# Optimization experiments

Measured on AMD Instinct MI355X. Metric: run time of the kernel, lower is better.

## Reference

```python
import jax, jax.numpy as jnp
import numpy as np

Bsz, L, D, N = 2, 2048, 1024, 16
LN_EPS = 1e-5


def setup_inputs() -> dict:
    key = jax.random.key(0)
    ks = jax.random.split(key, 5)
    # A_log initialized as in the module: -log(arange(1, N+1)) broadcast over D
    A_log = -jnp.broadcast_to(jnp.log(jnp.arange(1, N + 1, dtype=jnp.float32))[None, :], (D, N))
    return {
        "x": jax.random.normal(ks[0], (Bsz, L, D), jnp.float32),
        "W_dt": jax.random.normal(ks[1], (D, D), jnp.float32) * 0.02,
        "b_dt": jnp.zeros((D,), jnp.float32),
        "W_B": jax.random.normal(ks[2], (N, D), jnp.float32) * 0.02,
        "W_C": jax.random.normal(ks[3], (N, D), jnp.float32) * 0.02,
        "D_param": jnp.ones((D,), jnp.float32),
        "A_log": A_log,
        "gamma": jnp.ones((D,), jnp.float32),
        "beta": jnp.zeros((D,), jnp.float32),
    }


def reference(x, W_dt, b_dt, W_B, W_C, D_param, A_log, gamma, beta):
    residual = x
    # LayerNorm (biased variance, eps=1e-5)
    mu = jnp.mean(x, axis=-1, keepdims=True)
    var = jnp.var(x, axis=-1, keepdims=True)
    xn = (x - mu) * jax.lax.rsqrt(var + LN_EPS) * gamma + beta

    dt = jax.nn.softplus(xn @ W_dt.T + b_dt)          # (B, L, D)
    A = -jnp.exp(A_log)                                # (D, N)
    B_in = xn @ W_B.T                                  # (B, L, N)
    C_in = xn @ W_C.T                                  # (B, L, N)

    A_bar = jnp.exp(dt[..., None] * A)                 # (B, L, D, N)
    # B_bar[t] * x[t] fused: dt * B_in * xn -> (B, L, D, N)
    Bx = dt[..., None] * B_in[:, :, None, :] * xn[..., None]

    def step(h, inputs):
        a_t, bx_t, c_t = inputs                        # (B,D,N), (B,D,N), (B,N)
        h = a_t * h + bx_t                             # (B, D, N)
        y_t = jnp.einsum('bn,bdn->bd', c_t, h)         # (B, D)
        return h, y_t

    h0 = jnp.zeros((x.shape[0], D, N), x.dtype)
    _, ys = jax.lax.scan(
        step, h0,
        (jnp.transpose(A_bar, (1, 0, 2, 3)),
         jnp.transpose(Bx, (1, 0, 2, 3)),
         jnp.transpose(C_in, (1, 0, 2))))
    y = jnp.transpose(ys, (1, 0, 2)) + D_param * residual
    return y
```

## Files before the change

### kernel.cpp

```cpp
#include <hip/hip_runtime.h>
#include <cstddef>

#define Bsz 2
#define Lr  2048
#define Dr  1024
#define Nr  16
#define M_ROWS (Bsz*Lr)
#define NPAD   1088
#define CHUNK  16
#define NCH    (Lr/CHUNK)

#define BM 64
#define BN 64
#define BK 64
#define NK (Dr/BK)

typedef __attribute__((ext_vector_type(8))) __bf16 bf16x8;
typedef __attribute__((ext_vector_type(4))) float floatx4;

__device__ __forceinline__ unsigned short f2bf(float f) {
    unsigned u = __float_as_uint(f);
    u += 0x7fffu + ((u >> 16) & 1u);
    return (unsigned short)(u >> 16);
}

__device__ __forceinline__ float bf2f(unsigned short u) {
    return __uint_as_float(((unsigned)u) << 16);
}

__device__ __forceinline__ float softplus_f(float x) {
    if (x > 0.f) return x + __logf(1.f + __expf(-x));
    return __logf(1.f + __expf(x));
}

__device__ __forceinline__ void gload_lds16(const unsigned short* g, unsigned short* l) {
    __builtin_amdgcn_global_load_lds((const __attribute__((address_space(1))) void*)g,
                                     (__attribute__((address_space(3))) void*)l, 16, 0, 0);
}

__global__ __launch_bounds__(256) void ln_pack_kernel(const float* __restrict__ x,
                                                      const float* __restrict__ gamma,
                                                      const float* __restrict__ beta,
                                                      unsigned short* __restrict__ xnb,
                                                      const float* __restrict__ Wdt,
                                                      const float* __restrict__ WB,
                                                      const float* __restrict__ WC,
                                                      unsigned short* __restrict__ Wcat) {
    if (blockIdx.x >= M_ROWS) {
        int i = (blockIdx.x - M_ROWS) * 256 + threadIdx.x;
        int row = i >> 10;
        int col = i & 1023;
        float v;
        if (row < Dr)                 v = Wdt[i];
        else if (row < Dr + Nr)       v = WB[(row - Dr) * Dr + col];
        else if (row < Dr + 2*Nr)     v = WC[(row - Dr - Nr) * Dr + col];
        else                          v = 0.f;
        Wcat[i] = f2bf(v);
        return;
    }
    int row = blockIdx.x;
    int tid = threadIdx.x;
    const float4* xr = (const float4*)(x + (size_t)row * Dr);
    float4 v = xr[tid];
    float s  = v.x + v.y + v.z + v.w;
    float ss = v.x*v.x + v.y*v.y + v.z*v.z + v.w*v.w;
    #pragma unroll
    for (int off = 32; off > 0; off >>= 1) {
        s  += __shfl_down(s, off);
        ss += __shfl_down(ss, off);
    }
    __shared__ float red[8];
    int wid = tid >> 6;
    if ((tid & 63) == 0) { red[wid*2] = s; red[wid*2+1] = ss; }
    __syncthreads();
    if (tid == 0) {
        float S = 0.f, SS = 0.f;
        #pragma unroll
        for (int w = 0; w < 4; w++) { S += red[w*2]; SS += red[w*2+1]; }
        float mu  = S * (1.f/Dr);
        float var = SS * (1.f/Dr) - mu*mu;
        red[0] = mu;
        red[1] = rsqrtf(var + 1e-5f);
    }
    __syncthreads();
    float mu = red[0], rs = red[1];
    float4 g = ((const float4*)gamma)[tid], bt = ((const float4*)beta)[tid];
    float4 o;
    o.x = (v.x - mu) * rs * g.x + bt.x;
    o.y = (v.y - mu) * rs * g.y + bt.y;
    o.z = (v.z - mu) * rs * g.z + bt.z;
    o.w = (v.w - mu) * rs * g.w + bt.w;
    ushort4 ob;
    ob.x = f2bf(o.x); ob.y = f2bf(o.y); ob.z = f2bf(o.z); ob.w = f2bf(o.w);
    ((ushort4*)(xnb + (size_t)row * Dr))[tid] = ob;
}

__global__ __launch_bounds__(256) void gemm_kernel(const unsigned short* __restrict__ xnb,
                                                   const unsigned short* __restrict__ w,
                                                   const float* __restrict__ b_dt,
                                                   unsigned short* __restrict__ dt,
                                                   float* __restrict__ bin,
                                                   float* __restrict__ cin) {
    __shared__ unsigned short As[BM * BK];
    __shared__ unsigned short Bs[BN * BK];
    int tid  = threadIdx.x;
    int wave = tid >> 6;
    int lane = tid & 63;
    int lm   = lane & 15;
    int quad = lane >> 4;
    int bid  = blockIdx.x;
    int xcd  = bid & 7;
    int j0   = bid >> 3;
    int nt   = j0 % 17;
    int mt   = (j0 / 17) * 8 + xcd;
    int Mb = mt * BM;
    int Nb = nt * BN;
    int wm = (wave >> 1) * 32;
    int wn = (wave & 1)  * 32;
    int koff = (mt + nt) & (NK - 1);

    int r0 = tid >> 3,         cg0 = (tid & 7) ^ (r0 & 7);
    int r1 = (tid + 256) >> 3, cg1 = ((tid + 256) & 7) ^ (r1 & 7);
    const unsigned short* Ag0 = xnb + (size_t)(Mb + r0) * Dr + cg0 * 8;
    const unsigned short* Ag1 = xnb + (size_t)(Mb + r1) * Dr + cg1 * 8;
    const unsigned short* Bg0 = w   + (size_t)(Nb + r0) * Dr + cg0 * 8;
    const unsigned short* Bg1 = w   + (size_t)(Nb + r1) * Dr + cg1 * 8;
    unsigned short* Al0 = &As[(size_t)tid * 8];
    unsigned short* Al1 = &As[(size_t)(tid + 256) * 8];
    unsigned short* Bl0 = &Bs[(size_t)tid * 8];
    unsigned short* Bl1 = &Bs[(size_t)(tid + 256) * 8];

    floatx4 acc[2][2] = {};

    for (int kk = 0; kk < NK; kk++) {
        int k0 = ((kk + koff) & (NK - 1)) * BK;
        gload_lds16(Ag0 + k0, Al0);
        gload_lds16(Ag1 + k0, Al1);
        gload_lds16(Bg0 + k0, Bl0);
        gload_lds16(Bg1 + k0, Bl1);
        __syncthreads();
        #pragma unroll
        for (int s = 0; s < 2; s++) {
            int ra0 = wm + lm, ra1 = wm + 16 + lm;
            int rb0 = wn + lm, rb1 = wn + 16 + lm;
            int cg = s * 4 + quad;
            bf16x8 a0 = *(const bf16x8*)&As[ra0 * BK + ((cg ^ (ra0 & 7)) * 8)];
            bf16x8 a1 = *(const bf16x8*)&As[ra1 * BK + ((cg ^ (ra1 & 7)) * 8)];
            bf16x8 b0 = *(const bf16x8*)&Bs[rb0 * BK + ((cg ^ (rb0 & 7)) * 8)];
            bf16x8 b1 = *(const bf16x8*)&Bs[rb1 * BK + ((cg ^ (rb1 & 7)) * 8)];
            acc[0][0] = __builtin_amdgcn_mfma_f32_16x16x32_bf16(a0, b0, acc[0][0], 0, 0, 0);
            acc[0][1] = __builtin_amdgcn_mfma_f32_16x16x32_bf16(a0, b1, acc[0][1], 0, 0, 0);
            acc[1][0] = __builtin_amdgcn_mfma_f32_16x16x32_bf16(a1, b0, acc[1][0], 0, 0, 0);
            acc[1][1] = __builtin_amdgcn_mfma_f32_16x16x32_bf16(a1, b1, acc[1][1], 0, 0, 0);
        }
        __syncthreads();
    }

    #pragma unroll
    for (int i = 0; i < 2; i++) {
        int grow0 = Mb + wm + i * 16 + quad * 4;
        #pragma unroll
        for (int jj = 0; jj < 2; jj++) {
            int gcol = Nb + wn + jj * 16 + lm;
            #pragma unroll
            for (int r = 0; r < 4; r++) {
                float v = acc[i][jj][r];
                int row = grow0 + r;
                if (gcol < Dr) {
                    dt[(size_t)row * Dr + gcol] = f2bf(softplus_f(v + b_dt[gcol]));
                } else if (gcol < Dr + Nr) {
                    bin[(size_t)row * Nr + (gcol - Dr)] = v;
                } else if (gcol < Dr + 2*Nr) {
                    cin[(size_t)row * Nr + (gcol - Dr - Nr)] = v;
                }
            }
        }
    }
}

__global__ __launch_bounds__(256) void scan1_kernel(const unsigned short* __restrict__ dtb,
                                                    const unsigned short* __restrict__ xnb,
                                                    const float* __restrict__ bin,
                                                    const float* __restrict__ A_log,
                                                    unsigned short* __restrict__ Pws,
                                                    unsigned short* __restrict__ hendws) {
    int tid = threadIdx.x;
    int d  = blockIdx.x * 256 + tid;
    int ch = blockIdx.y;
    int b  = blockIdx.z;
    size_t rowbase = (size_t)b * Lr + ch * CHUNK;

    float ac[16];
    #pragma unroll
    for (int i = 0; i < 4; i++) {
        float4 t = ((const float4*)(A_log + (size_t)d * Nr))[i];
        ac[i*4+0] = -__expf(t.x);
        ac[i*4+1] = -__expf(t.y);
        ac[i*4+2] = -__expf(t.z);
        ac[i*4+3] = -__expf(t.w);
    }

    __shared__ float lb[CHUNK * Nr];
    lb[tid] = bin[rowbase * Nr + tid];
    __syncthreads();

    float dtv[CHUNK], xv[CHUNK];
    {
        const unsigned short* dtp = dtb + rowbase * Dr + d;
        const unsigned short* xp  = xnb + rowbase * Dr + d;
        #pragma unroll
        for (int t = 0; t < CHUNK; t++) {
            dtv[t] = bf2f(dtp[(size_t)t * Dr]);
            xv[t]  = bf2f(xp[(size_t)t * Dr]);
        }
    }

    float h[16];
    #pragma unroll
    for (int n = 0; n < 16; n++) h[n] = 0.f;
    float S = 0.f;

    #pragma unroll
    for (int t = 0; t < CHUNK; t++) {
        float dv = dtv[t];
        S += dv;
        float cm = dv * xv[t];
        const float4* br4 = (const float4*)(lb + t * Nr);
        float4 q0 = br4[0], q1 = br4[1], q2 = br4[2], q3 = br4[3];
        float bb[16] = {q0.x,q0.y,q0.z,q0.w, q1.x,q1.y,q1.z,q1.w,
                        q2.x,q2.y,q2.z,q2.w, q3.x,q3.y,q3.z,q3.w};
        #pragma unroll
        for (int n = 0; n < 16; n++)
            h[n] = __expf(dv * ac[n]) * h[n] + cm * bb[n];
    }

    size_t obase = ((size_t)(b * NCH + ch) * Nr) * Dr + d;
    #pragma unroll
    for (int n = 0; n < 16; n++) {
        Pws[obase + (size_t)n * Dr]    = f2bf(__expf(S * ac[n]));
        hendws[obase + (size_t)n * Dr] = f2bf(h[n]);
    }
}

__global__ __launch_bounds__(256) void combine_kernel(const unsigned short* __restrict__ Pws,
                                                      const unsigned short* __restrict__ hendws,
                                                      unsigned short* __restrict__ hinws) {
    int id = blockIdx.x * 256 + threadIdx.x;
    int b  = id >> 14;
    int dn = id & 16383;
    size_t base = ((size_t)b * NCH) * (Nr * Dr) + dn;
    float hin = 0.f;
    for (int cb = 0; cb < NCH; cb += 8) {
        float p[8], he[8];
        #pragma unroll
        for (int u = 0; u < 8; u++) {
            size_t idx = base + (size_t)(cb + u) * (Nr * Dr);
            p[u]  = bf2f(Pws[idx]);
            he[u] = bf2f(hendws[idx]);
        }
        #pragma unroll
        for (int u = 0; u < 8; u++) {
            size_t idx = base + (size_t)(cb + u) * (Nr * Dr);
            hinws[idx] = f2bf(hin);
            hin = p[u] * hin + he[u];
        }
    }
}

__global__ __launch_bounds__(256) void scan2_kernel(const unsigned short* __restrict__ dtb,
                                                    const unsigned short* __restrict__ xnb,
                                                    const float* __restrict__ bin,
                                                    const float* __restrict__ cin,
                                                    const float* __restrict__ A_log,
                                                    const unsigned short* __restrict__ hinws,
                                                    const float* __restrict__ x,
                                                    const float* __restrict__ Dp,
                                                    float* __restrict__ out) {
    int tid = threadIdx.x;
    int d  = blockIdx.x * 256 + tid;
    int ch = blockIdx.y;
    int b  = blockIdx.z;
    size_t rowbase = (size_t)b * Lr + ch * CHUNK;

    float ac[16];
    #pragma unroll
    for (int i = 0; i < 4; i++) {
        float4 t = ((const float4*)(A_log + (size_t)d * Nr))[i];
        ac[i*4+0] = -__expf(t.x);
        ac[i*4+1] = -__expf(t.y);
        ac[i*4+2] = -__expf(t.z);
        ac[i*4+3] = -__expf(t.w);
    }

    __shared__ float lb[CHUNK * Nr];
    __shared__ float lc[CHUNK * Nr];
    lb[tid] = bin[rowbase * Nr + tid];
    lc[tid] = cin[rowbase * Nr + tid];
    __syncthreads();

    float dtv[CHUNK], xv[CHUNK];
    {
        const unsigned short* dtp = dtb + rowbase * Dr + d;
        const unsigned short* xp  = xnb + rowbase * Dr + d;
        #pragma unroll
        for (int t = 0; t < CHUNK; t++) {
            dtv[t] = bf2f(dtp[(size_t)t * Dr]);
            xv[t]  = bf2f(xp[(size_t)t * Dr]);
        }
    }

    size_t obase = ((size_t)(b * NCH + ch) * Nr) * Dr + d;
    float h[16];
    #pragma unroll
    for (int n = 0; n < 16; n++) h[n] = bf2f(hinws[obase + (size_t)n * Dr]);

    float dp = Dp[d];
    const float* xr = x   + rowbase * Dr + d;
    float* op       = out + rowbase * Dr + d;

    for (int tb = 0; tb < CHUNK; tb += 4) {
        float xr4[4];
        #pragma unroll
        for (int u = 0; u < 4; u++) xr4[u] = xr[(size_t)(tb + u) * Dr];
        #pragma unroll
        for (int u = 0; u < 4; u++) {
            int t = tb + u;
            float dv = dtv[t];
            float cm = dv * xv[t];
            const float4* br4 = (const float4*)(lb + t * Nr);
            const float4* cr4 = (const float4*)(lc + t * Nr);
            float4 q0 = br4[0], q1 = br4[1], q2 = br4[2], q3 = br4[3];
            float4 r0 = cr4[0], r1 = cr4[1], r2 = cr4[2], r3 = cr4[3];
            float bb[16] = {q0.x,q0.y,q0.z,q0.w, q1.x,q1.y,q1.z,q1.w,
                            q2.x,q2.y,q2.z,q2.w, q3.x,q3.y,q3.z,q3.w};
            float cc[16] = {r0.x,r0.y,r0.z,r0.w, r1.x,r1.y,r1.z,r1.w,
                            r2.x,r2.y,r2.z,r2.w, r3.x,r3.y,r3.z,r3.w};
            float y = 0.f;
            #pragma unroll
            for (int n = 0; n < 16; n++) {
                h[n] = __expf(dv * ac[n]) * h[n] + cm * bb[n];
                y += cc[n] * h[n];
            }
            op[(size_t)t * Dr] = y + dp * xr4[u];
        }
    }
}

extern "C" void kernel_launch(void* const* d_in, const int* in_sizes, int n_in,
                              void* d_out, int out_size, void* d_ws, size_t ws_size,
                              hipStream_t stream) {
    const float* x      = (const float*)d_in[0];
    const float* W_dt   = (const float*)d_in[1];
    const float* b_dt   = (const float*)d_in[2];
    const float* W_B    = (const float*)d_in[3];
    const float* W_C    = (const float*)d_in[4];
    const float* Dparam = (const float*)d_in[5];
    const float* A_log  = (const float*)d_in[6];
    const float* gamma  = (const float*)d_in[7];
    const float* beta   = (const float*)d_in[8];
    float* out = (float*)d_out;

    char* ws = (char*)d_ws;
    unsigned short* xnb  = (unsigned short*)(ws);
    unsigned short* wcat = (unsigned short*)(ws + 8388608);
    unsigned short* dtb  = (unsigned short*)(ws + 10616832);
    float*          bin  = (float*)(ws + 19005440);
    float*          cin  = (float*)(ws + 19267584);
    unsigned short* Pws  = (unsigned short*)(ws + 19529728);
    unsigned short* hend = (unsigned short*)(ws + 27918336);
    unsigned short* hin  = (unsigned short*)(ws + 36306944);

    ln_pack_kernel<<<M_ROWS + (NPAD * Dr) / 256, 256, 0, stream>>>(
        x, gamma, beta, xnb, W_dt, W_B, W_C, wcat);
    gemm_kernel<<<(M_ROWS / BM) * (NPAD / BN), 256, 0, stream>>>(xnb, wcat, b_dt, dtb, bin, cin);
    dim3 sgrid(Dr / 256, NCH, Bsz);
    scan1_kernel<<<sgrid, 256, 0, stream>>>(dtb, xnb, bin, A_log, Pws, hend);
    combine_kernel<<<(Bsz * Dr * Nr) / 256, 256, 0, stream>>>(Pws, hend, hin);
    scan2_kernel<<<sgrid, 256, 0, stream>>>(dtb, xnb, bin, cin, A_log, hin, x, Dparam, out);
}
```

Measured before the change: 149.6 us.

## Enlarge GEMM M-tile and pass chunk dt sums instead of per-state decays

The GEMM tile height doubles so each wave computes a 64x32 output block, improving reuse of B-tile loads and halving the block count. The chunked scan now stores only the per-channel fp32 sum of dt per chunk instead of a bf16 decay for every state. The combine kernel recomputes the decay with an exp from A_log, cutting workspace traffic. In exchange, registers per thread rise in the GEMM and the combine kernel does extra exp work.

New measurement: 155.2 us. 1.04x slower.

```diff
diff --git a/kernel.cpp b/kernel.cpp
--- a/kernel.cpp
+++ b/kernel.cpp
@@ -10,7 +10,7 @@
 #define CHUNK  16
 #define NCH    (Lr/CHUNK)
 
-#define BM 64
+#define BM 128
 #define BN 64
 #define BK 64
 #define NK (Dr/BK)
@@ -115,49 +115,63 @@
     int mt   = (j0 / 17) * 8 + xcd;
     int Mb = mt * BM;
     int Nb = nt * BN;
-    int wm = (wave >> 1) * 32;
+    int wm = (wave >> 1) * 64;
     int wn = (wave & 1)  * 32;
     int koff = (mt + nt) & (NK - 1);
 
-    int r0 = tid >> 3,         cg0 = (tid & 7) ^ (r0 & 7);
-    int r1 = (tid + 256) >> 3, cg1 = ((tid + 256) & 7) ^ (r1 & 7);
-    const unsigned short* Ag0 = xnb + (size_t)(Mb + r0) * Dr + cg0 * 8;
-    const unsigned short* Ag1 = xnb + (size_t)(Mb + r1) * Dr + cg1 * 8;
-    const unsigned short* Bg0 = w   + (size_t)(Nb + r0) * Dr + cg0 * 8;
-    const unsigned short* Bg1 = w   + (size_t)(Nb + r1) * Dr + cg1 * 8;
-    unsigned short* Al0 = &As[(size_t)tid * 8];
-    unsigned short* Al1 = &As[(size_t)(tid + 256) * 8];
-    unsigned short* Bl0 = &Bs[(size_t)tid * 8];
-    unsigned short* Bl1 = &Bs[(size_t)(tid + 256) * 8];
-
-    floatx4 acc[2][2] = {};
+    const unsigned short* AgP[4];
+    unsigned short*       AlP[4];
+    #pragma unroll
+    for (int q = 0; q < 4; q++) {
+        int c = tid + 256 * q;
+        int r = c >> 3, cg = (c & 7) ^ (r & 7);
+        AgP[q] = xnb + (size_t)(Mb + r) * Dr + cg * 8;
+        AlP[q] = &As[(size_t)c * 8];
+    }
+    const unsigned short* BgP[2];
+    unsigned short*       BlP[2];
+    #pragma unroll
+    for (int q = 0; q < 2; q++) {
+        int c = tid + 256 * q;
+        int r = c >> 3, cg = (c & 7) ^ (r & 7);
+        BgP[q] = w + (size_t)(Nb + r) * Dr + cg * 8;
+        BlP[q] = &Bs[(size_t)c * 8];
+    }
+
+    floatx4 acc[4][2] = {};
 
     for (int kk = 0; kk < NK; kk++) {
         int k0 = ((kk + koff) & (NK - 1)) * BK;
-        gload_lds16(Ag0 + k0, Al0);
-        gload_lds16(Ag1 + k0, Al1);
-        gload_lds16(Bg0 + k0, Bl0);
-        gload_lds16(Bg1 + k0, Bl1);
+        #pragma unroll
+        for (int q = 0; q < 4; q++) gload_lds16(AgP[q] + k0, AlP[q]);
+        #pragma unroll
+        for (int q = 0; q < 2; q++) gload_lds16(BgP[q] + k0, BlP[q]);
         __syncthreads();
         #pragma unroll
         for (int s = 0; s < 2; s++) {
-            int ra0 = wm + lm, ra1 = wm + 16 + lm;
-            int rb0 = wn + lm, rb1 = wn + 16 + lm;
             int cg = s * 4 + quad;
-            bf16x8 a0 = *(const bf16x8*)&As[ra0 * BK + ((cg ^ (ra0 & 7)) * 8)];
-            bf16x8 a1 = *(const bf16x8*)&As[ra1 * BK + ((cg ^ (ra1 & 7)) * 8)];
-            bf16x8 b0 = *(const bf16x8*)&Bs[rb0 * BK + ((cg ^ (rb0 & 7)) * 8)];
-            bf16x8 b1 = *(const bf16x8*)&Bs[rb1 * BK + ((cg ^ (rb1 & 7)) * 8)];
-            acc[0][0] = __builtin_amdgcn_mfma_f32_16x16x32_bf16(a0, b0, acc[0][0], 0, 0, 0);
-            acc[0][1] = __builtin_amdgcn_mfma_f32_16x16x32_bf16(a0, b1, acc[0][1], 0, 0, 0);
-            acc[1][0] = __builtin_amdgcn_mfma_f32_16x16x32_bf16(a1, b0, acc[1][0], 0, 0, 0);
-            acc[1][1] = __builtin_amdgcn_mfma_f32_16x16x32_bf16(a1, b1, acc[1][1], 0, 0, 0);
+            bf16x8 a[4], b[2];
+            #pragma unroll
+            for (int i = 0; i < 4; i++) {
+                int r = wm + i * 16 + lm;
+                a[i] = *(const bf16x8*)&As[r * BK + ((cg ^ (r & 7)) * 8)];
+            }
+            #pragma unroll
+            for (int j = 0; j < 2; j++) {
+                int r = wn + j * 16 + lm;
+                b[j] = *(const bf16x8*)&Bs[r * BK + ((cg ^ (r & 7)) * 8)];
+            }
+            #pragma unroll
+            for (int i = 0; i < 4; i++)
+                #pragma unroll
+                for (int j = 0; j < 2; j++)
+                    acc[i][j] = __builtin_amdgcn_mfma_f32_16x16x32_bf16(a[i], b[j], acc[i][j], 0, 0, 0);
         }
         __syncthreads();
     }
 
     #pragma unroll
-    for (int i = 0; i < 2; i++) {
+    for (int i = 0; i < 4; i++) {
         int grow0 = Mb + wm + i * 16 + quad * 4;
         #pragma unroll
         for (int jj = 0; jj < 2; jj++) {
@@ -182,7 +196,7 @@
                                                     const unsigned short* __restrict__ xnb,
                                                     const float* __restrict__ bin,
                                                     const float* __restrict__ A_log,
-                                                    unsigned short* __restrict__ Pws,
+                                                    float* __restrict__ Sws,
                                                     unsigned short* __restrict__ hendws) {
     int tid = threadIdx.x;
     int d  = blockIdx.x * 256 + tid;
@@ -234,35 +248,38 @@
             h[n] = __expf(dv * ac[n]) * h[n] + cm * bb[n];
     }
 
+    Sws[(size_t)(b * NCH + ch) * Dr + d] = S;
     size_t obase = ((size_t)(b * NCH + ch) * Nr) * Dr + d;
     #pragma unroll
-    for (int n = 0; n < 16; n++) {
-        Pws[obase + (size_t)n * Dr]    = f2bf(__expf(S * ac[n]));
+    for (int n = 0; n < 16; n++)
         hendws[obase + (size_t)n * Dr] = f2bf(h[n]);
-    }
-}
-
-__global__ __launch_bounds__(256) void combine_kernel(const unsigned short* __restrict__ Pws,
+}
+
+__global__ __launch_bounds__(256) void combine_kernel(const float* __restrict__ Sws,
                                                       const unsigned short* __restrict__ hendws,
+                                                      const float* __restrict__ A_log,
                                                       unsigned short* __restrict__ hinws) {
     int id = blockIdx.x * 256 + threadIdx.x;
     int b  = id >> 14;
     int dn = id & 16383;
-    size_t base = ((size_t)b * NCH) * (Nr * Dr) + dn;
+    int n  = dn >> 10;
+    int d  = dn & 1023;
+    float ac = -__expf(A_log[d * Nr + n]);
+    size_t sbase = (size_t)b * NCH * Dr + d;
+    size_t base  = (size_t)b * NCH * (Nr * Dr) + dn;
     float hin = 0.f;
     for (int cb = 0; cb < NCH; cb += 8) {
-        float p[8], he[8];
+        float S8[8], he[8];
         #pragma unroll
         for (int u = 0; u < 8; u++) {
-            size_t idx = base + (size_t)(cb + u) * (Nr * Dr);
-            p[u]  = bf2f(Pws[idx]);
-            he[u] = bf2f(hendws[idx]);
+            S8[u] = Sws[sbase + (size_t)(cb + u) * Dr];
+            he[u] = bf2f(hendws[base + (size_t)(cb + u) * (Nr * Dr)]);
         }
         #pragma unroll
         for (int u = 0; u < 8; u++) {
             size_t idx = base + (size_t)(cb + u) * (Nr * Dr);
             hinws[idx] = f2bf(hin);
-            hin = p[u] * hin + he[u];
+            hin = __expf(S8[u] * ac) * hin + he[u];
         }
     }
 }
@@ -366,15 +383,15 @@
     unsigned short* dtb  = (unsigned short*)(ws + 10616832);
     float*          bin  = (float*)(ws + 19005440);
     float*          cin  = (float*)(ws + 19267584);
-    unsigned short* Pws  = (unsigned short*)(ws + 19529728);
-    unsigned short* hend = (unsigned short*)(ws + 27918336);
-    unsigned short* hin  = (unsigned short*)(ws + 36306944);
+    float*          Sws  = (float*)(ws + 19529728);
+    unsigned short* hend = (unsigned short*)(ws + 20578304);
+    unsigned short* hin  = (unsigned short*)(ws + 28966912);
 
     ln_pack_kernel<<<M_ROWS + (NPAD * Dr) / 256, 256, 0, stream>>>(
         x, gamma, beta, xnb, W_dt, W_B, W_C, wcat);
     gemm_kernel<<<(M_ROWS / BM) * (NPAD / BN), 256, 0, stream>>>(xnb, wcat, b_dt, dtb, bin, cin);
     dim3 sgrid(Dr / 256, NCH, Bsz);
-    scan1_kernel<<<sgrid, 256, 0, stream>>>(dtb, xnb, bin, A_log, Pws, hend);
-    combine_kernel<<<(Bsz * Dr * Nr) / 256, 256, 0, stream>>>(Pws, hend, hin);
+    scan1_kernel<<<sgrid, 256, 0, stream>>>(dtb, xnb, bin, A_log, Sws, hend);
+    combine_kernel<<<(Bsz * Dr * Nr) / 256, 256, 0, stream>>>(Sws, hend, A_log, hin);
     scan2_kernel<<<sgrid, 256, 0, stream>>>(dtb, xnb, bin, cin, A_log, hin, x, Dparam, out);
 }
```
